# Kernel optimization log

Measured on AMD Instinct MI355X. Metric: run time of the kernel, lower is better.

The kernel has to match this reference:

```python
import jax, jax.numpy as jnp
import numpy as np
import math

C = 128
N_HEAD = 4
GROUPS = 16
EPS = 1e-5


def group_norm(x, w, b):
    # x: [B, C, H, W]; GroupNorm over (C//G, H, W) within each group
    B, c, H, W = x.shape
    xg = x.reshape(B, GROUPS, c // GROUPS, H, W)
    mu = xg.mean(axis=(2, 3, 4), keepdims=True)
    var = xg.var(axis=(2, 3, 4), keepdims=True)  # biased, matches torch GroupNorm
    xn = ((xg - mu) / jnp.sqrt(var + EPS)).reshape(B, c, H, W)
    return xn * w[None, :, None, None] + b[None, :, None, None]


def conv1x1(x, w, b=None):
    # 1x1 conv == channel contraction. w: [O, C], x: [B, C, H, W]
    y = jnp.einsum('oc,bchw->bohw', w, x)
    if b is not None:
        y = y + b[None, :, None, None]
    return y


def split_qkv(qkv):
    # qkv: [B, 3C, H, W] -> q,k,v each [B, n_head, head_dim, H*W]
    B, _, H, W = qkv.shape
    d = C // N_HEAD
    qkv = qkv.reshape(B, N_HEAD, 3 * d, H * W)
    return qkv[:, :, :d], qkv[:, :, d:2 * d], qkv[:, :, 2 * d:]


def attend(q, k, v):
    # q,k,v: [B, n, d, HW]. Scale is 1/sqrt(C) (full channel), as in the source.
    attn = jnp.einsum('bndi,bndj->bnij', q, k) / math.sqrt(C)
    attn = jax.nn.softmax(attn, axis=-1)
    return jnp.einsum('bnij,bndj->bndi', attn, v)


def setup_inputs() -> dict:
    key = jax.random.key(0)
    ks = jax.random.split(key, 10)
    B, H, W = 1, 64, 64
    s = 1.0 / math.sqrt(C)
    return {
        'x_A': jax.random.normal(ks[0], (B, C, H, W), jnp.float32),
        'x_B': jax.random.normal(ks[1], (B, C, H, W), jnp.float32),
        'gnA_w': jnp.ones((C,), jnp.float32),
        'gnA_b': jnp.zeros((C,), jnp.float32),
        'qkvA_w': jax.random.normal(ks[2], (3 * C, C), jnp.float32) * s,
        'outA_w': jax.random.normal(ks[3], (C, C), jnp.float32) * s,
        'outA_b': jnp.zeros((C,), jnp.float32),
        'qkvB_w': jax.random.normal(ks[4], (3 * C, C), jnp.float32) * s,
        'outB_w': jax.random.normal(ks[5], (C, C), jnp.float32) * s,
        'outB_b': jnp.zeros((C,), jnp.float32),
    }


def reference(x_A, x_B, gnA_w, gnA_b, qkvA_w, outA_w, outA_b, qkvB_w, outB_w, outB_b):
    B, c, H, W = x_A.shape
    # Faithful to source: norm_A is applied to BOTH inputs (norm_B unused),
    # and the residual is the *normalized* tensor.
    xA_n = group_norm(x_A, gnA_w, gnA_b)
    xB_n = group_norm(x_B, gnA_w, gnA_b)

    qA, kA, vA = split_qkv(conv1x1(xA_n, qkvA_w))
    qB, kB, vB = split_qkv(conv1x1(xB_n, qkvB_w))

    oA = attend(qB, kA, vA).reshape(B, c, H, W)
    out_A = conv1x1(oA, outA_w, outA_b) + xA_n

    oB = attend(qA, kB, vB).reshape(B, c, H, W)
    out_B = conv1x1(oB, outB_w, outB_b) + xB_n
    return (out_A, out_B)
```

## Files before the change

### kernel.cpp

```cpp
#include <hip/hip_runtime.h>
#include <hip/hip_bf16.h>

using short8 = __attribute__((ext_vector_type(8))) short;
using s16x4  = __attribute__((ext_vector_type(4))) short;
using f32x4  = __attribute__((ext_vector_type(4))) float;
using int4v  = __attribute__((ext_vector_type(4))) int;

#define HW 4096
#define CC 128
#define DH 32
#define NH 4

__device__ inline float bf2f(unsigned short u) {
    unsigned int x = ((unsigned int)u) << 16;
    return __builtin_bit_cast(float, x);
}
__device__ inline unsigned short f2bf(float f) {
    unsigned int x = __builtin_bit_cast(unsigned int, f);
    unsigned int lsb = (x >> 16) & 1u;
    x += 0x7fffu + lsb;
    return (unsigned short)(x >> 16);
}
__device__ inline float ldf(const void* p, size_t i, bool f32) {
    return f32 ? ((const float*)p)[i] : bf2f(((const unsigned short*)p)[i]);
}
__device__ inline float fexp2(float x) { return __builtin_amdgcn_exp2f(x); }
__device__ inline short8 pack8(const float* e) {
    int4v p;
#pragma unroll
    for (int t = 0; t < 4; t++) {
        unsigned lo = __builtin_bit_cast(unsigned, e[2 * t])     >> 16;
        unsigned hi = __builtin_bit_cast(unsigned, e[2 * t + 1]) & 0xffff0000u;
        p[t] = (int)(lo | hi);
    }
    return __builtin_bit_cast(short8, p);
}
__device__ inline bool detect_f32(const void* xA) {
    unsigned int w = ((const unsigned int*)xA)[threadIdx.x & 63];
    float a = fabsf(bf2f((unsigned short)(w & 0xffffu)));
    bool bad = !(a >= 1e-6f && a <= 1e4f);
    return __popcll(__ballot(bad)) > 32;
}

__global__ void prep_kernel(const void* __restrict__ xA, const void* __restrict__ xB,
                            const void* __restrict__ qA, const void* __restrict__ qB,
                            const void* __restrict__ oA, const void* __restrict__ oB,
                            const void* __restrict__ bA, const void* __restrict__ bB,
                            float* __restrict__ raw2,
                            unsigned short* __restrict__ Wc) {
    const bool f32 = detect_f32(xA);
    const int b = blockIdx.x;
    if (b < 256) {
        const int s = b >> 7, c = b & 127;
        const void* x = s ? xB : xA;
        float sum = 0.f, sumsq = 0.f;
        for (int p = threadIdx.x; p < HW; p += 256) {
            float v = ldf(x, (size_t)c * HW + p, f32);
            sum += v; sumsq += v * v;
        }
        for (int off = 32; off; off >>= 1) {
            sum   += __shfl_down(sum, off);
            sumsq += __shfl_down(sumsq, off);
        }
        __shared__ float smem[8];
        int w = threadIdx.x >> 6;
        if ((threadIdx.x & 63) == 0) { smem[w] = sum; smem[4 + w] = sumsq; }
        __syncthreads();
        if (threadIdx.x == 0) {
            raw2[(s * 128 + c) * 2]     = smem[0] + smem[1] + smem[2] + smem[3];
            raw2[(s * 128 + c) * 2 + 1] = smem[4] + smem[5] + smem[6] + smem[7];
        }
    } else {
        for (int i = (b - 256) * 256 + threadIdx.x; i < 131328; i += 64 * 256) {
            const void* s; int off;
            if      (i < 49152)  { s = qA; off = i; }
            else if (i < 98304)  { s = qB; off = i - 49152; }
            else if (i < 114688) { s = oA; off = i - 98304; }
            else if (i < 131072) { s = oB; off = i - 114688; }
            else if (i < 131200) { s = bA; off = i - 131072; }
            else                 { s = bB; off = i - 131200; }
            Wc[i] = f2bf(ldf(s, off, f32));
        }
    }
}

__global__ void gn_apply(const void* __restrict__ xA, const void* __restrict__ xB,
                         const void* __restrict__ gw, const void* __restrict__ gb,
                         const float* __restrict__ raw2,
                         unsigned short* __restrict__ xn) {
    const bool f32 = detect_f32(xA);
    const int s = blockIdx.y;
    const int p0 = blockIdx.x * 32;
    const void* x = s ? xB : xA;
    const int tid = threadIdx.x;
    __shared__ float st[16][2];
    __shared__ float tile[128][33];
    if (tid < 16) {
        float s1 = 0.f, s2 = 0.f;
#pragma unroll
        for (int c = 0; c < 8; c++) {
            s1 += raw2[(s * 128 + tid * 8 + c) * 2];
            s2 += raw2[(s * 128 + tid * 8 + c) * 2 + 1];
        }
        const float NEL = 8.0f * HW;
        float mu = s1 / NEL;
        float var = s2 / NEL - mu * mu;
        st[tid][0] = mu;
        st[tid][1] = rsqrtf(var + 1e-5f);
    }
    __syncthreads();
    const int pl = tid & 31;
#pragma unroll
    for (int cc = 0; cc < 16; cc++) {
        int c = cc * 8 + (tid >> 5);
        float v = ldf(x, (size_t)c * HW + p0 + pl, f32);
        tile[c][pl] = (v - st[c >> 3][0]) * st[c >> 3][1] * ldf(gw, c, f32)
                    + ldf(gb, c, f32);
    }
    __syncthreads();
    unsigned int* xo = (unsigned int*)(xn + (size_t)s * HW * CC);
#pragma unroll
    for (int k = 0; k < 8; k++) {
        int idx = tid + k * 256;
        int p = idx >> 6, c2 = idx & 63;
        unsigned lo = (unsigned)f2bf(tile[2 * c2][p]);
        unsigned hi = (unsigned)f2bf(tile[2 * c2 + 1][p]);
        xo[((size_t)(p0 + p) * CC >> 1) + c2] = lo | (hi << 16);
    }
}

__global__ void qkv_kernel(const unsigned short* __restrict__ Wc,
                           const unsigned short* __restrict__ xn,
                           unsigned short* __restrict__ Kt,
                           unsigned short* __restrict__ Vp) {
    const int z = blockIdx.z;
    const unsigned short* Wq = Wc + (size_t)z * 49152;
    const int o0 = blockIdx.x * 16;
    const int w = threadIdx.x >> 6, lane = threadIdx.x & 63;
    const int quad = lane >> 4, col = lane & 15;
    const int p0 = blockIdx.y * 64 + w * 16;
    const unsigned short* xb = xn + (size_t)z * HW * CC;
    f32x4 acc = {0.f, 0.f, 0.f, 0.f};
#pragma unroll
    for (int kc = 0; kc < 4; kc++) {
        short8 a = *(const short8*)(Wq + (size_t)(o0 + col) * CC + kc * 32 + quad * 8);
        short8 b = *(const short8*)(xb + (size_t)(p0 + col) * CC + kc * 32 + quad * 8);
        acc = __builtin_amdgcn_mfma_f32_16x16x32_bf16(a, b, acc, 0, 0, 0);
    }
#pragma unroll
    for (int r = 0; r < 4; r++) {
        int o = o0 + quad * 4 + r;
        int h = o / 96, rr = o % 96;
        int p = p0 + col;
        unsigned short vb = f2bf(acc[r]);
        if (rr >= 32 && rr < 64) {
            Kt[((size_t)(z * NH + h) * HW + p) * DH + (rr - 32)] = vb;
        } else if (rr >= 64) {
            int d = rr - 64;
            int jb = p >> 6, jl = p & 63;
            int sub = jl >> 5, jm = jl & 31;
            int qp, jj;
            if (jm < 16) { qp = jm >> 2; jj = jm & 3; }
            else         { qp = (jm - 16) >> 2; jj = 4 + ((jm - 16) & 3); }
            int frag  = (d >> 4) + sub * 2;
            int lanep = qp * 16 + (d & 15);
            Vp[(((size_t)(z * NH + h) * 64 + jb) * 2048)
               + frag * 512 + lanep * 8 + jj] = vb;
        }
    }
}

__global__ __launch_bounds__(512, 4) void attn_kernel(
        const unsigned short* __restrict__ Wc,
        const unsigned short* __restrict__ xn,
        const unsigned short* __restrict__ Kt_all,
        const unsigned short* __restrict__ Vp_all,
        unsigned short* __restrict__ OT_all) {
    const int z = blockIdx.z, h = blockIdx.y;
    const int tid = threadIdx.x;
    const int wave = tid >> 6, lane = tid & 63;
    const int quad = lane >> 4, col = lane & 15;
    const int sc = wave;
    const int zq = 1 - z;
    const unsigned short* Kt = Kt_all + (size_t)(z * NH + h) * HW * DH;
    const unsigned short* Vp = Vp_all + (size_t)(z * NH + h) * 64 * 2048;
    unsigned short* OT = OT_all + (size_t)z * HW * CC;

    const int i0 = blockIdx.x * 32;

    __shared__ __align__(16) short qlds[32][40];
    __shared__ float ldsO[8][2][32][17];
    __shared__ float ldsl[8][32];

    if (wave < 4) {
        const float kscale = 0.12751569782174257f;
        const int stq = wave >> 1, dcq = wave & 1;
        const unsigned short* Wq = Wc + (size_t)zq * 49152 + (size_t)(96 * h) * CC;
        const unsigned short* xq = xn + (size_t)zq * HW * CC;
        f32x4 qa = {0.f, 0.f, 0.f, 0.f};
#pragma unroll
        for (int kc = 0; kc < 4; kc++) {
            short8 a = *(const short8*)(Wq + (size_t)(dcq * 16 + col) * CC + kc * 32 + quad * 8);
            short8 b = *(const short8*)(xq + (size_t)(i0 + stq * 16 + col) * CC + kc * 32 + quad * 8);
            qa = __builtin_amdgcn_mfma_f32_16x16x32_bf16(a, b, qa, 0, 0, 0);
        }
#pragma unroll
        for (int r = 0; r < 4; r++)
            qlds[stq * 16 + col][dcq * 16 + quad * 4 + r] = (short)f2bf(qa[r] * kscale);
    }
    __syncthreads();

    f32x4 acc0[2], acc1[2];
    float li[2];
#pragma unroll
    for (int s = 0; s < 2; s++) {
        acc0[s] = (f32x4){0.f, 0.f, 0.f, 0.f};
        acc1[s] = (f32x4){0.f, 0.f, 0.f, 0.f};
        li[s] = 0.f;
    }

    const int jb = sc * 512;
    for (int j0 = jb; j0 < jb + 512; j0 += 64) {
        short8 kf[4];
#pragma unroll
        for (int X = 0; X < 4; X++)
            kf[X] = *(const short8*)(Kt + (size_t)(j0 + X * 16 + col) * DH + quad * 8);
        const unsigned short* vb_ = Vp + (size_t)(j0 >> 6) * 2048 + lane * 8;
        short8 va0 = *(const short8*)(vb_);
        short8 va1 = *(const short8*)(vb_ + 512);
        short8 va2 = *(const short8*)(vb_ + 1024);
        short8 va3 = *(const short8*)(vb_ + 1536);
#pragma unroll
        for (int s = 0; s < 2; s++) {
            short8 qf = *(const short8*)(&qlds[s * 16 + col][quad * 8]);
            f32x4 zero = {0.f, 0.f, 0.f, 0.f};
            f32x4 st0 = __builtin_amdgcn_mfma_f32_16x16x32_bf16(kf[0], qf, zero, 0, 0, 0);
            f32x4 st1 = __builtin_amdgcn_mfma_f32_16x16x32_bf16(kf[1], qf, zero, 0, 0, 0);
            f32x4 st2 = __builtin_amdgcn_mfma_f32_16x16x32_bf16(kf[2], qf, zero, 0, 0, 0);
            f32x4 st3 = __builtin_amdgcn_mfma_f32_16x16x32_bf16(kf[3], qf, zero, 0, 0, 0);
            float e[16], l0 = 0.f, l1 = 0.f;
#pragma unroll
            for (int r = 0; r < 4; r++) {
                e[r]      = fexp2(st0[r]);
                e[4 + r]  = fexp2(st1[r]);
                e[8 + r]  = fexp2(st2[r]);
                e[12 + r] = fexp2(st3[r]);
                l0 += e[r] + e[4 + r];
                l1 += e[8 + r] + e[12 + r];
            }
            li[s] += l0 + l1;
            short8 pb0 = pack8(&e[0]);
            short8 pb1 = pack8(&e[8]);
            acc0[s] = __builtin_amdgcn_mfma_f32_16x16x32_bf16(va0, pb0, acc0[s], 0, 0, 0);
            acc1[s] = __builtin_amdgcn_mfma_f32_16x16x32_bf16(va1, pb0, acc1[s], 0, 0, 0);
            acc0[s] = __builtin_amdgcn_mfma_f32_16x16x32_bf16(va2, pb1, acc0[s], 0, 0, 0);
            acc1[s] = __builtin_amdgcn_mfma_f32_16x16x32_bf16(va3, pb1, acc1[s], 0, 0, 0);
        }
    }
#pragma unroll
    for (int s = 0; s < 2; s++) {
        li[s] += __shfl_xor(li[s], 16);
        li[s] += __shfl_xor(li[s], 32);
#pragma unroll
        for (int r = 0; r < 4; r++) {
            ldsO[sc][s][quad * 4 + r][col]      = acc0[s][r];
            ldsO[sc][s][16 + quad * 4 + r][col] = acc1[s][r];
        }
        if (quad == 0) ldsl[sc][s * 16 + col] = li[s];
    }
    __syncthreads();
#pragma unroll
    for (int k = 0; k < 2; k++) {
        int idx = tid + k * 512;
        int il = idx >> 5, d = idx & 31;
        int itc = il >> 4, cc2 = il & 15;
        float L = 0.f, O = 0.f;
#pragma unroll
        for (int c8 = 0; c8 < 8; c8++) {
            L += ldsl[c8][il];
            O += ldsO[c8][itc][d][cc2];
        }
        OT[(size_t)(i0 + il) * CC + h * DH + d] = f2bf(O / L);
    }
}

__global__ void proj_kernel(const unsigned short* __restrict__ Wc,
                            const unsigned short* __restrict__ OT_all,
                            const void* __restrict__ xA,
                            const void* __restrict__ xB,
                            const void* __restrict__ gw,
                            const void* __restrict__ gb,
                            const float* __restrict__ raw2,
                            float* __restrict__ out) {
    const bool f32 = detect_f32(xA);
    const int z = blockIdx.z;
    const unsigned short* Wp = Wc + 98304 + (size_t)z * 16384;
    const unsigned short* bp = Wc + 131072 + (size_t)z * 128;
    const void* xz = z ? xB : xA;
    const int tid = threadIdx.x;
    __shared__ float st[16][2];
    if (tid < 16) {
        float s1 = 0.f, s2 = 0.f;
#pragma unroll
        for (int c = 0; c < 8; c++) {
            s1 += raw2[(z * 128 + tid * 8 + c) * 2];
            s2 += raw2[(z * 128 + tid * 8 + c) * 2 + 1];
        }
        const float NEL = 8.0f * HW;
        float mu = s1 / NEL;
        float var = s2 / NEL - mu * mu;
        st[tid][0] = mu;
        st[tid][1] = rsqrtf(var + 1e-5f);
    }
    __syncthreads();
    const int o0 = blockIdx.x * 16;
    const int w = tid >> 6, lane = tid & 63;
    const int quad = lane >> 4, col = lane & 15;
    const int p0 = blockIdx.y * 64 + w * 16;
    const unsigned short* ob = OT_all + (size_t)z * HW * CC;
    f32x4 acc = {0.f, 0.f, 0.f, 0.f};
#pragma unroll
    for (int kc = 0; kc < 4; kc++) {
        short8 a = *(const short8*)(Wp + (size_t)(o0 + col) * CC + kc * 32 + quad * 8);
        short8 b = *(const short8*)(ob + (size_t)(p0 + col) * CC + kc * 32 + quad * 8);
        acc = __builtin_amdgcn_mfma_f32_16x16x32_bf16(a, b, acc, 0, 0, 0);
    }
    const int p = p0 + col;
#pragma unroll
    for (int r = 0; r < 4; r++) {
        int o = o0 + quad * 4 + r;
        float xv = ldf(xz, (size_t)o * HW + p, f32);
        float res = (xv - st[o >> 3][0]) * st[o >> 3][1] * ldf(gw, o, f32)
                  + ldf(gb, o, f32);
        out[(size_t)z * CC * HW + (size_t)o * HW + p] = acc[r] + bf2f(bp[o]) + res;
    }
}

extern "C" void kernel_launch(void* const* d_in, const int* in_sizes, int n_in,
                              void* d_out, int out_size, void* d_ws, size_t ws_size,
                              hipStream_t stream) {
    (void)in_sizes; (void)n_in; (void)out_size; (void)ws_size;
    const void* xA    = d_in[0];
    const void* xB    = d_in[1];
    const void* gnw   = d_in[2];
    const void* gnb   = d_in[3];
    const void* qkvAw = d_in[4];
    const void* outAw = d_in[5];
    const void* outAb = d_in[6];
    const void* qkvBw = d_in[7];
    const void* outBw = d_in[8];
    const void* outBb = d_in[9];

    char* ws = (char*)d_ws;
    float*          raw2 = (float*)(ws);
    unsigned short* Wc   = (unsigned short*)(ws + 4096);
    unsigned short* Kt   = (unsigned short*)(ws + (1u << 20));
    unsigned short* Vp   = (unsigned short*)(ws + (3u << 20));
    unsigned short* OT   = (unsigned short*)(ws + (5u << 20));
    unsigned short* xn   = (unsigned short*)(ws + (7u << 20));

    prep_kernel<<<320, 256, 0, stream>>>(xA, xB, qkvAw, qkvBw, outAw, outBw,
                                         outAb, outBb, raw2, Wc);
    gn_apply<<<dim3(128, 2), 256, 0, stream>>>(xA, xB, gnw, gnb, raw2, xn);
    qkv_kernel<<<dim3(24, 64, 2), 256, 0, stream>>>(Wc, xn, Kt, Vp);
    attn_kernel<<<dim3(128, NH, 2), 512, 0, stream>>>(Wc, xn, Kt, Vp, OT);
    proj_kernel<<<dim3(8, 64, 2), 256, 0, stream>>>(Wc, OT, xA, xB, gnw, gnb,
                                                    raw2, (float*)d_out);
}
```

Baseline: 141.1 us.

## Fuse GroupNorm apply with K/V projection using an LDS tile

Merges the groupnorm-apply kernel and the QKV projection kernel into one kernel. Each block normalizes 16 pixels, writes xn to global memory, and also stores the bf16 tile in LDS. It then computes only the K and V output tiles with MFMA directly from LDS, skipping the Q rows since attention recomputes Q from xn. This saves a kernel launch and the global re-read of xn. The trade-off is less parallelism per projection and weight reloads from global memory in every block.

```diff
diff --git a/kernel.cpp b/kernel.cpp
--- a/kernel.cpp
+++ b/kernel.cpp
@@ -84,23 +84,27 @@
     }
 }
 
-__global__ void gn_apply(const void* __restrict__ xA, const void* __restrict__ xB,
-                         const void* __restrict__ gw, const void* __restrict__ gb,
-                         const float* __restrict__ raw2,
-                         unsigned short* __restrict__ xn) {
+__global__ void gnqkv_kernel(const void* __restrict__ xA, const void* __restrict__ xB,
+                             const void* __restrict__ gw, const void* __restrict__ gb,
+                             const float* __restrict__ raw2,
+                             const unsigned short* __restrict__ Wc,
+                             unsigned short* __restrict__ xn,
+                             unsigned short* __restrict__ Kt,
+                             unsigned short* __restrict__ Vp) {
     const bool f32 = detect_f32(xA);
-    const int s = blockIdx.y;
-    const int p0 = blockIdx.x * 32;
-    const void* x = s ? xB : xA;
+    const int z = blockIdx.y;
+    const int p0 = blockIdx.x * 16;
+    const void* x = z ? xB : xA;
     const int tid = threadIdx.x;
     __shared__ float st[16][2];
-    __shared__ float tile[128][33];
+    __shared__ float tile[128][17];
+    __shared__ __align__(16) unsigned int btile[16][68];
     if (tid < 16) {
         float s1 = 0.f, s2 = 0.f;
 #pragma unroll
         for (int c = 0; c < 8; c++) {
-            s1 += raw2[(s * 128 + tid * 8 + c) * 2];
-            s2 += raw2[(s * 128 + tid * 8 + c) * 2 + 1];
+            s1 += raw2[(z * 128 + tid * 8 + c) * 2];
+            s2 += raw2[(z * 128 + tid * 8 + c) * 2 + 1];
         }
         const float NEL = 8.0f * HW;
         float mu = s1 / NEL;
@@ -109,63 +113,63 @@
         st[tid][1] = rsqrtf(var + 1e-5f);
     }
     __syncthreads();
-    const int pl = tid & 31;
-#pragma unroll
-    for (int cc = 0; cc < 16; cc++) {
-        int c = cc * 8 + (tid >> 5);
+    const int pl = tid & 15;
+#pragma unroll
+    for (int it = 0; it < 8; it++) {
+        int c = it * 16 + (tid >> 4);
         float v = ldf(x, (size_t)c * HW + p0 + pl, f32);
         tile[c][pl] = (v - st[c >> 3][0]) * st[c >> 3][1] * ldf(gw, c, f32)
                     + ldf(gb, c, f32);
     }
     __syncthreads();
-    unsigned int* xo = (unsigned int*)(xn + (size_t)s * HW * CC);
-#pragma unroll
-    for (int k = 0; k < 8; k++) {
+    unsigned int* xo = (unsigned int*)(xn + (size_t)z * HW * CC);
+#pragma unroll
+    for (int k = 0; k < 4; k++) {
         int idx = tid + k * 256;
         int p = idx >> 6, c2 = idx & 63;
         unsigned lo = (unsigned)f2bf(tile[2 * c2][p]);
         unsigned hi = (unsigned)f2bf(tile[2 * c2 + 1][p]);
-        xo[((size_t)(p0 + p) * CC >> 1) + c2] = lo | (hi << 16);
-    }
-}
-
-__global__ void qkv_kernel(const unsigned short* __restrict__ Wc,
-                           const unsigned short* __restrict__ xn,
-                           unsigned short* __restrict__ Kt,
-                           unsigned short* __restrict__ Vp) {
-    const int z = blockIdx.z;
+        unsigned pr = lo | (hi << 16);
+        xo[(size_t)(p0 + p) * 64 + c2] = pr;
+        btile[p][c2] = pr;
+    }
+    __syncthreads();
+    const int wave = tid >> 6, lane = tid & 63;
+    const int quad = lane >> 4, col = lane & 15;
     const unsigned short* Wq = Wc + (size_t)z * 49152;
-    const int o0 = blockIdx.x * 16;
-    const int w = threadIdx.x >> 6, lane = threadIdx.x & 63;
-    const int quad = lane >> 4, col = lane & 15;
-    const int p0 = blockIdx.y * 64 + w * 16;
-    const unsigned short* xb = xn + (size_t)z * HW * CC;
-    f32x4 acc = {0.f, 0.f, 0.f, 0.f};
-#pragma unroll
-    for (int kc = 0; kc < 4; kc++) {
-        short8 a = *(const short8*)(Wq + (size_t)(o0 + col) * CC + kc * 32 + quad * 8);
-        short8 b = *(const short8*)(xb + (size_t)(p0 + col) * CC + kc * 32 + quad * 8);
-        acc = __builtin_amdgcn_mfma_f32_16x16x32_bf16(a, b, acc, 0, 0, 0);
-    }
-#pragma unroll
-    for (int r = 0; r < 4; r++) {
-        int o = o0 + quad * 4 + r;
-        int h = o / 96, rr = o % 96;
-        int p = p0 + col;
-        unsigned short vb = f2bf(acc[r]);
-        if (rr >= 32 && rr < 64) {
-            Kt[((size_t)(z * NH + h) * HW + p) * DH + (rr - 32)] = vb;
-        } else if (rr >= 64) {
-            int d = rr - 64;
-            int jb = p >> 6, jl = p & 63;
-            int sub = jl >> 5, jm = jl & 31;
-            int qp, jj;
-            if (jm < 16) { qp = jm >> 2; jj = jm & 3; }
-            else         { qp = (jm - 16) >> 2; jj = 4 + ((jm - 16) & 3); }
-            int frag  = (d >> 4) + sub * 2;
-            int lanep = qp * 16 + (d & 15);
-            Vp[(((size_t)(z * NH + h) * 64 + jb) * 2048)
-               + frag * 512 + lanep * 8 + jj] = vb;
+    const unsigned short* bt = (const unsigned short*)btile;
+#pragma unroll
+    for (int i = 0; i < 4; i++) {
+        int idx = wave * 4 + i;
+        int h = idx >> 2;
+        int o0 = (6 * h + 2 + (idx & 3)) * 16;
+        f32x4 acc = {0.f, 0.f, 0.f, 0.f};
+#pragma unroll
+        for (int kc = 0; kc < 4; kc++) {
+            short8 a = *(const short8*)(Wq + (size_t)(o0 + col) * CC + kc * 32 + quad * 8);
+            short8 b = *(const short8*)(bt + col * 136 + kc * 32 + quad * 8);
+            acc = __builtin_amdgcn_mfma_f32_16x16x32_bf16(a, b, acc, 0, 0, 0);
+        }
+#pragma unroll
+        for (int r = 0; r < 4; r++) {
+            int o = o0 + quad * 4 + r;
+            int rr = o % 96;
+            int p = p0 + col;
+            unsigned short vb = f2bf(acc[r]);
+            if (rr < 64) {
+                Kt[((size_t)(z * NH + h) * HW + p) * DH + (rr - 32)] = vb;
+            } else {
+                int d = rr - 64;
+                int jb = p >> 6, jl = p & 63;
+                int sub = jl >> 5, jm = jl & 31;
+                int qp, jj;
+                if (jm < 16) { qp = jm >> 2; jj = jm & 3; }
+                else         { qp = (jm - 16) >> 2; jj = 4 + ((jm - 16) & 3); }
+                int frag  = (d >> 4) + sub * 2;
+                int lanep = qp * 16 + (d & 15);
+                Vp[(((size_t)(z * NH + h) * 64 + jb) * 2048)
+                   + frag * 512 + lanep * 8 + jj] = vb;
+            }
         }
     }
 }
@@ -361,8 +365,8 @@
 
     prep_kernel<<<320, 256, 0, stream>>>(xA, xB, qkvAw, qkvBw, outAw, outBw,
                                          outAb, outBb, raw2, Wc);
-    gn_apply<<<dim3(128, 2), 256, 0, stream>>>(xA, xB, gnw, gnb, raw2, xn);
-    qkv_kernel<<<dim3(24, 64, 2), 256, 0, stream>>>(Wc, xn, Kt, Vp);
+    gnqkv_kernel<<<dim3(256, 2), 256, 0, stream>>>(xA, xB, gnw, gnb, raw2, Wc,
+                                                   xn, Kt, Vp);
     attn_kernel<<<dim3(128, NH, 2), 512, 0, stream>>>(Wc, xn, Kt, Vp, OT);
     proj_kernel<<<dim3(8, 64, 2), 256, 0, stream>>>(Wc, OT, xA, xB, gnw, gnb,
                                                     raw2, (float*)d_out);
```

New measurement: 129.1 us. 1.09x faster.
